# Optimization experiments

Hardware: AMD Instinct MI355X
Metric: run time of the kernel (lower is better)

## Reference

```python
import jax, jax.numpy as jnp
import numpy as np

N_SRC, N_DST, E, D, H = 100000, 10000, 320000, 128, 128
LN_EPS = 1e-5


def setup_inputs() -> dict:
    key = jax.random.key(0)
    ks = jax.random.split(key, 12)
    h_src = jax.random.normal(ks[0], (N_SRC, D), jnp.float32)
    h_dst = jax.random.normal(ks[1], (N_DST, D), jnp.float32)
    s_emb = jax.random.normal(ks[2], (N_DST, D), jnp.float32)
    edge_weight = jax.random.uniform(ks[3], (E,), jnp.float32)
    src_idx = jax.random.randint(ks[4], (E,), 0, N_SRC)
    dst_idx = jnp.sort(jax.random.randint(ks[5], (E,), 0, N_DST))
    # session_attention: Linear(2D->H, no bias) -> tanh -> Linear(H->1, no bias)
    W1 = jax.random.normal(ks[6], (2 * D, H), jnp.float32) / np.sqrt(2 * D)
    w2 = jax.random.normal(ks[7], (H,), jnp.float32) / np.sqrt(H)
    # output_proj: Linear(2D->D) with bias
    Wo = jax.random.normal(ks[8], (2 * D, D), jnp.float32) / np.sqrt(2 * D)
    bo = jnp.zeros((D,), jnp.float32)
    gamma = jnp.ones((D,), jnp.float32)
    beta = jnp.zeros((D,), jnp.float32)
    return {"h_src": h_src, "h_dst": h_dst, "s_emb": s_emb,
            "edge_weight": edge_weight, "src_idx": src_idx, "dst_idx": dst_idx,
            "W1": W1, "w2": w2, "Wo": Wo, "bo": bo, "gamma": gamma, "beta": beta}


def reference(h_src, h_dst, s_emb, edge_weight, src_idx, dst_idx, W1, w2, Wo, bo, gamma, beta):
    d = h_src.shape[1]
    # concat([h_src[src], s_emb[dst]]) @ W1 == h_src[src] @ W1[:d] + s_emb[dst] @ W1[d:]
    # project per-node first (cheaper than per-edge concat matmul)
    p_src = h_src @ W1[:d]          # [N_src, H]
    p_dst = s_emb @ W1[d:]          # [N_dst, H]
    raw = jnp.tanh(p_src[src_idx] + p_dst[dst_idx]) @ w2   # [E]
    raw = raw * edge_weight
    # edge_softmax: segment softmax over incoming edges of each dst node
    seg_max = jax.ops.segment_max(raw, dst_idx, num_segments=h_dst.shape[0])
    seg_max = jnp.where(jnp.isfinite(seg_max), seg_max, 0.0)  # handle degree-0 dsts
    ex = jnp.exp(raw - seg_max[dst_idx])
    den = jax.ops.segment_sum(ex, dst_idx, num_segments=h_dst.shape[0])
    attn = ex / den[dst_idx]                                 # [E]
    # u_mul_e + sum: weighted gather-scatter aggregation
    h_global = jax.ops.segment_sum(h_src[src_idx] * attn[:, None], dst_idx,
                                   num_segments=h_dst.shape[0])  # [N_dst, D]
    # output_proj on concat([h_dst, h_global])
    out = h_dst @ Wo[:d] + h_global @ Wo[d:] + bo
    # residual + layer norm (dropout = identity in eval)
    x = h_dst + out
    mu = jnp.mean(x, axis=-1, keepdims=True)
    var = jnp.mean((x - mu) ** 2, axis=-1, keepdims=True)
    y = (x - mu) / jnp.sqrt(var + LN_EPS) * gamma + beta
    return (y, attn[:, None])
```

## Files before the change

kernel.cpp:

```cpp
#include <hip/hip_runtime.h>
#include <math.h>

#define D128 128
#define SCAPW 256

typedef unsigned int uint32;
typedef unsigned short ushort_t;
typedef short bf16x8 __attribute__((ext_vector_type(8)));
typedef float f32x4 __attribute__((ext_vector_type(4)));
typedef float f32x2 __attribute__((ext_vector_type(2)));

__device__ __forceinline__ ushort_t bf16_of(float x) {
  uint32 u = __float_as_uint(x);
  return (ushort_t)((u + 0x7fffu + ((u >> 16) & 1u)) >> 16);
}
__device__ __forceinline__ uint32 pack_bf2(float x, float y) {
  uint32 bx = __float_as_uint(x);
  uint32 by = __float_as_uint(y);
  bx = (bx + 0x7fffu + ((bx >> 16) & 1u)) >> 16;
  by = (by + 0x7fffu + ((by >> 16) & 1u)) & 0xffff0000u;
  return bx | by;
}

__device__ __forceinline__ float fast_tanh(float x) {
  float e = __expf(2.0f * x);
  float r = __builtin_amdgcn_rcpf(1.0f + e);
  return fmaf(-2.0f, r, 1.0f);
}

__device__ __forceinline__ uint32 pack_fp8x4(float a, float b, float c, float d) {
  int u = __builtin_amdgcn_cvt_pk_fp8_f32(a, b, 0, false);
  u = __builtin_amdgcn_cvt_pk_fp8_f32(c, d, u, true);
  return (uint32)u;
}

__device__ __forceinline__ bf16x8 bf16x8_of(float4 a, float4 c) {
  union { uint4 u; bf16x8 h; } r;
  r.u.x = pack_bf2(a.x, a.y);
  r.u.y = pack_bf2(a.z, a.w);
  r.u.z = pack_bf2(c.x, c.y);
  r.u.w = pack_bf2(c.z, c.w);
  return r.h;
}

__device__ __forceinline__ float score8(uint2 us, f32x2 pd0, f32x2 pd1, f32x2 pd2,
                                        f32x2 pd3, float4 wA, float4 wB) {
  f32x2 a0 = __builtin_amdgcn_cvt_pk_f32_fp8(us.x, false);
  f32x2 a1 = __builtin_amdgcn_cvt_pk_f32_fp8(us.x, true);
  f32x2 a2 = __builtin_amdgcn_cvt_pk_f32_fp8(us.y, false);
  f32x2 a3 = __builtin_amdgcn_cvt_pk_f32_fp8(us.y, true);
  float sc;
  sc = fast_tanh(a0.x + pd0.x) * wA.x;
  sc = fmaf(fast_tanh(a0.y + pd0.y), wA.y, sc);
  sc = fmaf(fast_tanh(a1.x + pd1.x), wA.z, sc);
  sc = fmaf(fast_tanh(a1.y + pd1.y), wA.w, sc);
  sc = fmaf(fast_tanh(a2.x + pd2.x), wB.x, sc);
  sc = fmaf(fast_tanh(a2.y + pd2.y), wB.y, sc);
  sc = fmaf(fast_tanh(a3.x + pd3.x), wB.z, sc);
  sc = fmaf(fast_tanh(a3.y + pd3.y), wB.w, sc);
  return sc;
}

__global__ __launch_bounds__(256) void prep_all(
    const float* __restrict__ W1, const float* __restrict__ Wo,
    const int* __restrict__ dst_idx,
    ushort_t* __restrict__ Wfrag, ushort_t* __restrict__ Wo_frag,
    int* __restrict__ off, int E, int N) {
  const int b = blockIdx.x;
  const int tid = threadIdx.x;
  if (b < 16) {
    int t = b * 256 + tid;
    int lane = t & 63;
    int kc = (t >> 6) & 3;
    int nt = (t >> 8) & 7;
    int h = (t >> 11) & 1;
    int m = lane & 15;
    int quad = lane >> 4;
    int krow = h * D128 + kc * 32 + quad * 8;
    int ncol = nt * 16 + m;
    ushort_t fr[8];
#pragma unroll
    for (int j = 0; j < 8; j++) fr[j] = bf16_of(W1[(size_t)(krow + j) * D128 + ncol]);
    *(uint4*)(Wfrag + (size_t)t * 8) = *(const uint4*)fr;
  } else if (b < 32) {
    int t = (b - 16) * 256 + tid;
    int lane = t & 63;
    int kc = (t >> 6) & 7;
    int nt = (t >> 9) & 7;
    int m = lane & 15;
    int quad = lane >> 4;
    int krow = kc * 32 + quad * 8;
    int ncol = nt * 16 + m;
    ushort_t fr[8];
#pragma unroll
    for (int j = 0; j < 8; j++) fr[j] = bf16_of(Wo[(size_t)(krow + j) * D128 + ncol]);
    *(uint4*)(Wo_frag + (size_t)t * 8) = *(const uint4*)fr;
  } else {
    int e = (b - 32) * 256 + tid;
    if (e >= E) return;
    int d = dst_idx[e];
    int dprev = (e == 0) ? -1 : dst_idx[e - 1];
    for (int v = dprev + 1; v <= d; v++) off[v] = e;
    if (e == E - 1) {
      for (int v = d + 1; v <= N; v++) off[v] = E;
    }
  }
}

__global__ __launch_bounds__(256) void gemm_mfma(
    const float* __restrict__ Xa, const float* __restrict__ Xb,
    const ushort_t* __restrict__ Wfrag,
    uint32* __restrict__ Pa, uint32* __restrict__ Pb,
    uint32* __restrict__ x_f8,
    int Ma, int Mb, int nblk_a) {
  __shared__ uint4 WL[2048];
  const int blk = blockIdx.x;
  const float* X;
  const uint4* Wg;
  uint32* P;
  int M, row0;
  bool emit8;
  if (blk < nblk_a) {
    X = Xa; P = Pa; Wg = (const uint4*)Wfrag;             M = Ma; row0 = blk * 64; emit8 = true;
  } else {
    X = Xb; P = Pb; Wg = (const uint4*)(Wfrag + 16384);   M = Mb; row0 = (blk - nblk_a) * 64; emit8 = false;
  }

  const int tid = threadIdx.x;
  const int wave = tid >> 6;
  const int lane = tid & 63;
  const int m = lane & 15;
  const int quad = lane >> 4;

  const int ra = min(row0 + wave * 16 + m, M - 1);
  const float* xp = X + (size_t)ra * D128 + quad * 8;

  float4 xf[8];
#pragma unroll
  for (int kc = 0; kc < 4; kc++) {
    xf[kc * 2]     = *(const float4*)(xp + kc * 32);
    xf[kc * 2 + 1] = *(const float4*)(xp + kc * 32 + 4);
  }

  uint4 wtmp[8];
#pragma unroll
  for (int j = 0; j < 8; j++) wtmp[j] = Wg[tid + 256 * j];
#pragma unroll
  for (int j = 0; j < 8; j++) WL[tid + 256 * j] = wtmp[j];

  if (emit8) {
#pragma unroll
    for (int kc = 0; kc < 4; kc++) {
      uint2 q;
      q.x = pack_fp8x4(xf[kc * 2].x, xf[kc * 2].y, xf[kc * 2].z, xf[kc * 2].w);
      q.y = pack_fp8x4(xf[kc * 2 + 1].x, xf[kc * 2 + 1].y, xf[kc * 2 + 1].z, xf[kc * 2 + 1].w);
      *(uint2*)(x_f8 + (size_t)ra * 32 + kc * 8 + quad * 2) = q;
    }
  }
  bf16x8 xb[4];
#pragma unroll
  for (int kc = 0; kc < 4; kc++) xb[kc] = bf16x8_of(xf[kc * 2], xf[kc * 2 + 1]);

  __syncthreads();

  f32x4 acc[8];
#pragma unroll
  for (int nt = 0; nt < 8; nt++) acc[nt] = (f32x4){0.f, 0.f, 0.f, 0.f};

#pragma unroll
  for (int kc = 0; kc < 4; kc++) {
#pragma unroll
    for (int nt = 0; nt < 8; nt++) {
      bf16x8 wf = *(const bf16x8*)&WL[(nt * 4 + kc) * 64 + lane];
      acc[nt] = __builtin_amdgcn_mfma_f32_16x16x32_bf16(wf, xb[kc], acc[nt], 0, 0, 0);
    }
  }

  __syncthreads();
  uint32* Ys = (uint32*)WL;
#pragma unroll
  for (int nt = 0; nt < 8; nt++)
    Ys[(wave * 16 + m) * 36 + nt * 4 + quad] =
        pack_fp8x4(acc[nt][0], acc[nt][1], acc[nt][2], acc[nt][3]);
  __syncthreads();

#pragma unroll
  for (int it = 0; it < 2; it++) {
    int f = tid + 256 * it;
    int row = f >> 3;
    int cu = (f & 7) * 4;
    int grow = row0 + row;
    if (grow < M) *(uint4*)(P + (size_t)grow * 32 + cu) = *(const uint4*)(&Ys[row * 36 + cu]);
  }
}

__global__ __launch_bounds__(256) void attn_agg_kernel(
    const uint32* __restrict__ p_src_f8, const uint32* __restrict__ p_dst_f8,
    const float* __restrict__ w2, const float* __restrict__ ew,
    const int* __restrict__ src_idx, const int* __restrict__ off,
    const uint32* __restrict__ h_src_f8,
    float* __restrict__ attn_out, uint32* __restrict__ h_glob_bf, int N_dst) {
  const int tid = threadIdx.x;
  const int wv = tid >> 6;
  const int lane = tid & 63;
  const int v = blockIdx.x * 4 + wv;

  __shared__ float sex[4][SCAPW];
  __shared__ int ssrc[4][SCAPW];
  if (v >= N_dst) return;

  const int lo = off[v], hi = off[v + 1];
  const int deg = hi - lo;
  const int sub = lane & 15;
  const int eg = lane >> 4;
  const bool fast = (deg <= SCAPW);

  float4 wA = *(const float4*)(w2 + sub * 8);
  float4 wB = *(const float4*)(w2 + sub * 8 + 4);
  uint2 pdu = *(const uint2*)(p_dst_f8 + (size_t)v * 32 + sub * 2);
  f32x2 pd0 = __builtin_amdgcn_cvt_pk_f32_fp8(pdu.x, false);
  f32x2 pd1 = __builtin_amdgcn_cvt_pk_f32_fp8(pdu.x, true);
  f32x2 pd2 = __builtin_amdgcn_cvt_pk_f32_fp8(pdu.y, false);
  f32x2 pd3 = __builtin_amdgcn_cvt_pk_f32_fp8(pdu.y, true);

  float den = 0.f;
  for (int base = 0; base < deg; base += 8) {
    const int ei0 = base + eg;
    const int ei1 = base + 4 + eg;
    const bool v0 = ei0 < deg;
    const bool v1 = ei1 < deg;
    int s0 = 0, s1 = 0;
    float ew0 = 0.f, ew1 = 0.f;
    uint2 us0, us1;
    us0.x = us0.y = us1.x = us1.y = 0u;
    if (v0) {
      const int e = lo + ei0;
      s0 = src_idx[e];
      ew0 = ew[e];
      us0 = *(const uint2*)(p_src_f8 + (size_t)s0 * 32 + sub * 2);
    }
    if (v1) {
      const int e = lo + ei1;
      s1 = src_idx[e];
      ew1 = ew[e];
      us1 = *(const uint2*)(p_src_f8 + (size_t)s1 * 32 + sub * 2);
    }
    float ex0 = 0.f, ex1 = 0.f;
    if (v0) {
      float sc = score8(us0, pd0, pd1, pd2, pd3, wA, wB);
#pragma unroll
      for (int o = 1; o <= 8; o <<= 1) sc += __shfl_xor(sc, o, 64);
      ex0 = __expf(sc * ew0);
      if (sub == 0) {
        if (fast) { sex[wv][ei0] = ex0; ssrc[wv][ei0] = s0; }
        else attn_out[lo + ei0] = ex0;
      }
    }
    if (v1) {
      float sc = score8(us1, pd0, pd1, pd2, pd3, wA, wB);
#pragma unroll
      for (int o = 1; o <= 8; o <<= 1) sc += __shfl_xor(sc, o, 64);
      ex1 = __expf(sc * ew1);
      if (sub == 0) {
        if (fast) { sex[wv][ei1] = ex1; ssrc[wv][ei1] = s1; }
        else attn_out[lo + ei1] = ex1;
      }
    }
    den += (sub == 0) ? (ex0 + ex1) : 0.f;
  }
#pragma unroll
  for (int o = 1; o <= 32; o <<= 1) den += __shfl_xor(den, o, 64);
  const float inv = (deg > 0) ? 1.0f / den : 0.0f;

  const int c4 = lane & 31;
  const int hw = lane >> 5;
  float a0 = 0.f, a1 = 0.f, a2 = 0.f, a3 = 0.f;

  if (fast) {
    const int pad = (deg + 15) & ~15;
    for (int i = deg + lane; i < pad; i += 64) { sex[wv][i] = 0.f; ssrc[wv][i] = 0; }
    for (int i = lane; i < deg; i += 64) attn_out[lo + i] = sex[wv][i] * inv;
    for (int b = 0; b < pad; b += 16) {
#pragma unroll
      for (int j = 0; j < 8; j++) {
        const int idx = b + j * 2 + hw;
        float ex = sex[wv][idx];
        int s = ssrc[wv][idx];
        uint32 u = h_src_f8[(size_t)s * 32 + c4];
        f32x2 h0 = __builtin_amdgcn_cvt_pk_f32_fp8(u, false);
        f32x2 h1 = __builtin_amdgcn_cvt_pk_f32_fp8(u, true);
        a0 = fmaf(ex, h0.x, a0);
        a1 = fmaf(ex, h0.y, a1);
        a2 = fmaf(ex, h1.x, a2);
        a3 = fmaf(ex, h1.y, a3);
      }
    }
  } else {
    for (int b = 0; b < deg; b += 16) {
#pragma unroll
      for (int j = 0; j < 8; j++) {
        const int idx = b + j * 2 + hw;
        float ex = 0.f;
        int s = 0;
        if (idx < deg) { ex = attn_out[lo + idx]; s = src_idx[lo + idx]; }
        uint32 u = h_src_f8[(size_t)s * 32 + c4];
        f32x2 h0 = __builtin_amdgcn_cvt_pk_f32_fp8(u, false);
        f32x2 h1 = __builtin_amdgcn_cvt_pk_f32_fp8(u, true);
        a0 = fmaf(ex, h0.x, a0);
        a1 = fmaf(ex, h0.y, a1);
        a2 = fmaf(ex, h1.x, a2);
        a3 = fmaf(ex, h1.y, a3);
      }
    }
    for (int i = lane; i < deg; i += 64) attn_out[lo + i] *= inv;
  }

  a0 += __shfl_xor(a0, 32, 64);
  a1 += __shfl_xor(a1, 32, 64);
  a2 += __shfl_xor(a2, 32, 64);
  a3 += __shfl_xor(a3, 32, 64);
  if (hw == 0) {
    uint2 o;
    o.x = pack_bf2(a0 * inv, a1 * inv);
    o.y = pack_bf2(a2 * inv, a3 * inv);
    *(uint2*)(h_glob_bf + (size_t)v * 64 + c4 * 2) = o;
  }
}

__global__ __launch_bounds__(128) void out_mfma_ln(
    const float* __restrict__ h_dst, const ushort_t* __restrict__ h_glob_bf,
    const ushort_t* __restrict__ Wo_frag,
    const float* __restrict__ bo,
    const float* __restrict__ gamma, const float* __restrict__ beta,
    float* __restrict__ y, int N) {
  __shared__ float sbo[128], sgam[128], sbet[128];
  const int tid = threadIdx.x;
  if (tid < 128) { sbo[tid] = bo[tid]; sgam[tid] = gamma[tid]; sbet[tid] = beta[tid]; }
  __syncthreads();

  const int w = tid >> 6;
  const int lane = tid & 63;
  const int m = lane & 15;
  const int quad = lane >> 4;
  const int row0 = blockIdx.x * 32 + w * 16;
  const int ra = min(row0 + m, N - 1);
  const bf16x8* Wf = (const bf16x8*)Wo_frag;

  float4 f0[4], f1[4];
  bf16x8 ag[4];
#pragma unroll
  for (int kc = 0; kc < 4; kc++) {
    const float* p = h_dst + (size_t)ra * D128 + kc * 32 + quad * 8;
    f0[kc] = *(const float4*)p;
    f1[kc] = *(const float4*)(p + 4);
  }
#pragma unroll
  for (int kc = 0; kc < 4; kc++)
    ag[kc] = *(const bf16x8*)(h_glob_bf + (size_t)ra * D128 + kc * 32 + quad * 8);

  f32x4 acc[8];
#pragma unroll
  for (int nt = 0; nt < 8; nt++) acc[nt] = (f32x4){0.f, 0.f, 0.f, 0.f};

#pragma unroll
  for (int kc = 0; kc < 8; kc++) {
    bf16x8 a = (kc < 4) ? bf16x8_of(f0[kc & 3], f1[kc & 3]) : ag[kc & 3];
#pragma unroll
    for (int nt = 0; nt < 8; nt++) {
      bf16x8 bfr = Wf[(nt * 8 + kc) * 64 + lane];
      acc[nt] = __builtin_amdgcn_mfma_f32_16x16x32_bf16(a, bfr, acc[nt], 0, 0, 0);
    }
  }

#pragma unroll
  for (int r = 0; r < 4; r++) {
    const int grow = row0 + quad * 4 + r;
    const int gr = min(grow, N - 1);
    float x[8];
    float s1 = 0.f, s2 = 0.f;
#pragma unroll
    for (int nt = 0; nt < 8; nt++) {
      float hd = h_dst[(size_t)gr * D128 + nt * 16 + m];
      float xv = hd + acc[nt][r] + sbo[nt * 16 + m];
      x[nt] = xv;
      s1 += xv;
      s2 = fmaf(xv, xv, s2);
    }
#pragma unroll
    for (int o = 1; o <= 8; o <<= 1) {
      s1 += __shfl_xor(s1, o, 64);
      s2 += __shfl_xor(s2, o, 64);
    }
    float mu = s1 * (1.0f / 128.0f);
    float var = s2 * (1.0f / 128.0f) - mu * mu;
    float rstd = __builtin_amdgcn_rcpf(sqrtf(var + 1e-5f));
    if (grow < N) {
#pragma unroll
      for (int nt = 0; nt < 8; nt++) {
        int c = nt * 16 + m;
        y[(size_t)grow * D128 + c] = (x[nt] - mu) * rstd * sgam[c] + sbet[c];
      }
    }
  }
}

extern "C" void kernel_launch(void* const* d_in, const int* in_sizes, int n_in,
                              void* d_out, int out_size, void* d_ws, size_t ws_size,
                              hipStream_t stream) {
  const float* h_src = (const float*)d_in[0];
  const float* h_dst = (const float*)d_in[1];
  const float* s_emb = (const float*)d_in[2];
  const float* ew    = (const float*)d_in[3];
  const int* src_idx = (const int*)d_in[4];
  const int* dst_idx = (const int*)d_in[5];
  const float* W1    = (const float*)d_in[6];
  const float* w2    = (const float*)d_in[7];
  const float* Wo    = (const float*)d_in[8];
  const float* bo    = (const float*)d_in[9];
  const float* gamma = (const float*)d_in[10];
  const float* beta  = (const float*)d_in[11];

  const int N_src = in_sizes[0] / D128;
  const int N_dst = in_sizes[1] / D128;
  const int E = in_sizes[3];

  float* out_y = (float*)d_out;
  float* out_attn = out_y + (size_t)N_dst * D128;

  uint32* p_src_f8 = (uint32*)d_ws;
  uint32* p_dst_f8 = p_src_f8 + (size_t)N_src * 32;
  uint32* h_src_f8 = p_dst_f8 + (size_t)N_dst * 32;
  uint32* h_glob_bf = h_src_f8 + (size_t)N_src * 32;
  int* seg_off = (int*)(h_glob_bf + (size_t)N_dst * 64);
  ushort_t* Wfrag = (ushort_t*)(seg_off + N_dst + 1 + 3);
  ushort_t* Wo_frag = Wfrag + 32768;

  const int nblk_a = (N_src + 63) / 64;
  const int nblk_b = (N_dst + 63) / 64;
  const int nb_seg = (E + 255) / 256;

  prep_all<<<32 + nb_seg, 256, 0, stream>>>(
      W1, Wo, dst_idx, Wfrag, Wo_frag, seg_off, E, N_dst);
  gemm_mfma<<<nblk_a + nblk_b, 256, 0, stream>>>(
      h_src, s_emb, Wfrag, p_src_f8, p_dst_f8, h_src_f8, N_src, N_dst, nblk_a);
  attn_agg_kernel<<<(N_dst + 3) / 4, 256, 0, stream>>>(
      p_src_f8, p_dst_f8, w2, ew, src_idx, seg_off, h_src_f8, out_attn,
      h_glob_bf, N_dst);
  out_mfma_ln<<<(N_dst + 31) / 32, 128, 0, stream>>>(
      h_dst, (const ushort_t*)h_glob_bf, Wo_frag,
      bo, gamma, beta, out_y, N_dst);
}
```

Baseline: 163.0 us.

## Split edge scoring into edge-parallel kernel and stage Wo fragments in LDS

Edge attention scoring moves out of the per-destination aggregation kernel into a separate edge-parallel kernel, so that load balance no longer depends on node degree. The aggregation kernel then reads the exp scores back from global memory to form the denominator and weighted sum. This adds one kernel launch and an extra round trip of the scores through global memory. Separately, the output projection now uses 256-thread blocks that stage the two halves of the Wo fragments in shared memory, with the fragment layout reordered to match.

```diff
diff --git a/kernel.cpp b/kernel.cpp
--- a/kernel.cpp
+++ b/kernel.cpp
@@ -2,7 +2,6 @@
 #include <math.h>
 
 #define D128 128
-#define SCAPW 256
 
 typedef unsigned int uint32;
 typedef unsigned short ushort_t;
@@ -43,21 +42,24 @@
   return r.h;
 }
 
-__device__ __forceinline__ float score8(uint2 us, f32x2 pd0, f32x2 pd1, f32x2 pd2,
-                                        f32x2 pd3, float4 wA, float4 wB) {
+__device__ __forceinline__ float score8_raw(uint2 us, uint2 ud, float4 wA, float4 wB) {
   f32x2 a0 = __builtin_amdgcn_cvt_pk_f32_fp8(us.x, false);
   f32x2 a1 = __builtin_amdgcn_cvt_pk_f32_fp8(us.x, true);
   f32x2 a2 = __builtin_amdgcn_cvt_pk_f32_fp8(us.y, false);
   f32x2 a3 = __builtin_amdgcn_cvt_pk_f32_fp8(us.y, true);
+  f32x2 d0 = __builtin_amdgcn_cvt_pk_f32_fp8(ud.x, false);
+  f32x2 d1 = __builtin_amdgcn_cvt_pk_f32_fp8(ud.x, true);
+  f32x2 d2 = __builtin_amdgcn_cvt_pk_f32_fp8(ud.y, false);
+  f32x2 d3 = __builtin_amdgcn_cvt_pk_f32_fp8(ud.y, true);
   float sc;
-  sc = fast_tanh(a0.x + pd0.x) * wA.x;
-  sc = fmaf(fast_tanh(a0.y + pd0.y), wA.y, sc);
-  sc = fmaf(fast_tanh(a1.x + pd1.x), wA.z, sc);
-  sc = fmaf(fast_tanh(a1.y + pd1.y), wA.w, sc);
-  sc = fmaf(fast_tanh(a2.x + pd2.x), wB.x, sc);
-  sc = fmaf(fast_tanh(a2.y + pd2.y), wB.y, sc);
-  sc = fmaf(fast_tanh(a3.x + pd3.x), wB.z, sc);
-  sc = fmaf(fast_tanh(a3.y + pd3.y), wB.w, sc);
+  sc = fast_tanh(a0.x + d0.x) * wA.x;
+  sc = fmaf(fast_tanh(a0.y + d0.y), wA.y, sc);
+  sc = fmaf(fast_tanh(a1.x + d1.x), wA.z, sc);
+  sc = fmaf(fast_tanh(a1.y + d1.y), wA.w, sc);
+  sc = fmaf(fast_tanh(a2.x + d2.x), wB.x, sc);
+  sc = fmaf(fast_tanh(a2.y + d2.y), wB.y, sc);
+  sc = fmaf(fast_tanh(a3.x + d3.x), wB.z, sc);
+  sc = fmaf(fast_tanh(a3.y + d3.y), wB.w, sc);
   return sc;
 }
 
@@ -85,11 +87,12 @@
   } else if (b < 32) {
     int t = (b - 16) * 256 + tid;
     int lane = t & 63;
-    int kc = (t >> 6) & 7;
-    int nt = (t >> 9) & 7;
+    int kc4 = (t >> 6) & 3;
+    int nt = (t >> 8) & 7;
+    int half = (t >> 11) & 1;
     int m = lane & 15;
     int quad = lane >> 4;
-    int krow = kc * 32 + quad * 8;
+    int krow = (half * 4 + kc4) * 32 + quad * 8;
     int ncol = nt * 16 + m;
     ushort_t fr[8];
 #pragma unroll
@@ -194,9 +197,47 @@
   }
 }
 
-__global__ __launch_bounds__(256) void attn_agg_kernel(
+__global__ __launch_bounds__(256) void score_kernel(
     const uint32* __restrict__ p_src_f8, const uint32* __restrict__ p_dst_f8,
     const float* __restrict__ w2, const float* __restrict__ ew,
+    const int* __restrict__ src_idx, const int* __restrict__ dst_idx,
+    float* __restrict__ ex_out, int E) {
+  const int tid = threadIdx.x;
+  const int wv = tid >> 6;
+  const int lane = tid & 63;
+  const int sub = lane & 15;
+  const int eg = lane >> 4;
+  const int wbase = (blockIdx.x * 4 + wv) * 64;
+  if (wbase >= E) return;
+
+  const float4 wA = *(const float4*)(w2 + sub * 8);
+  const float4 wB = *(const float4*)(w2 + sub * 8 + 4);
+
+  for (int i0 = 0; i0 < 64; i0 += 16) {
+    int e[4];
+    uint2 us[4], ud[4];
+    float ewv[4];
+#pragma unroll
+    for (int j = 0; j < 4; j++) {
+      e[j] = wbase + i0 + j * 4 + eg;
+      const int ee = min(e[j], E - 1);
+      const int s = src_idx[ee];
+      const int d = dst_idx[ee];
+      ewv[j] = ew[ee];
+      us[j] = *(const uint2*)(p_src_f8 + (size_t)s * 32 + sub * 2);
+      ud[j] = *(const uint2*)(p_dst_f8 + (size_t)d * 32 + sub * 2);
+    }
+#pragma unroll
+    for (int j = 0; j < 4; j++) {
+      float sc = score8_raw(us[j], ud[j], wA, wB);
+#pragma unroll
+      for (int o = 1; o <= 8; o <<= 1) sc += __shfl_xor(sc, o, 64);
+      if (sub == 0 && e[j] < E) ex_out[e[j]] = __expf(sc * ewv[j]);
+    }
+  }
+}
+
+__global__ __launch_bounds__(256) void agg_kernel(
     const int* __restrict__ src_idx, const int* __restrict__ off,
     const uint32* __restrict__ h_src_f8,
     float* __restrict__ attn_out, uint32* __restrict__ h_glob_bf, int N_dst) {
@@ -204,70 +245,13 @@
   const int wv = tid >> 6;
   const int lane = tid & 63;
   const int v = blockIdx.x * 4 + wv;
-
-  __shared__ float sex[4][SCAPW];
-  __shared__ int ssrc[4][SCAPW];
   if (v >= N_dst) return;
 
   const int lo = off[v], hi = off[v + 1];
   const int deg = hi - lo;
-  const int sub = lane & 15;
-  const int eg = lane >> 4;
-  const bool fast = (deg <= SCAPW);
-
-  float4 wA = *(const float4*)(w2 + sub * 8);
-  float4 wB = *(const float4*)(w2 + sub * 8 + 4);
-  uint2 pdu = *(const uint2*)(p_dst_f8 + (size_t)v * 32 + sub * 2);
-  f32x2 pd0 = __builtin_amdgcn_cvt_pk_f32_fp8(pdu.x, false);
-  f32x2 pd1 = __builtin_amdgcn_cvt_pk_f32_fp8(pdu.x, true);
-  f32x2 pd2 = __builtin_amdgcn_cvt_pk_f32_fp8(pdu.y, false);
-  f32x2 pd3 = __builtin_amdgcn_cvt_pk_f32_fp8(pdu.y, true);
 
   float den = 0.f;
-  for (int base = 0; base < deg; base += 8) {
-    const int ei0 = base + eg;
-    const int ei1 = base + 4 + eg;
-    const bool v0 = ei0 < deg;
-    const bool v1 = ei1 < deg;
-    int s0 = 0, s1 = 0;
-    float ew0 = 0.f, ew1 = 0.f;
-    uint2 us0, us1;
-    us0.x = us0.y = us1.x = us1.y = 0u;
-    if (v0) {
-      const int e = lo + ei0;
-      s0 = src_idx[e];
-      ew0 = ew[e];
-      us0 = *(const uint2*)(p_src_f8 + (size_t)s0 * 32 + sub * 2);
-    }
-    if (v1) {
-      const int e = lo + ei1;
-      s1 = src_idx[e];
-      ew1 = ew[e];
-      us1 = *(const uint2*)(p_src_f8 + (size_t)s1 * 32 + sub * 2);
-    }
-    float ex0 = 0.f, ex1 = 0.f;
-    if (v0) {
-      float sc = score8(us0, pd0, pd1, pd2, pd3, wA, wB);
-#pragma unroll
-      for (int o = 1; o <= 8; o <<= 1) sc += __shfl_xor(sc, o, 64);
-      ex0 = __expf(sc * ew0);
-      if (sub == 0) {
-        if (fast) { sex[wv][ei0] = ex0; ssrc[wv][ei0] = s0; }
-        else attn_out[lo + ei0] = ex0;
-      }
-    }
-    if (v1) {
-      float sc = score8(us1, pd0, pd1, pd2, pd3, wA, wB);
-#pragma unroll
-      for (int o = 1; o <= 8; o <<= 1) sc += __shfl_xor(sc, o, 64);
-      ex1 = __expf(sc * ew1);
-      if (sub == 0) {
-        if (fast) { sex[wv][ei1] = ex1; ssrc[wv][ei1] = s1; }
-        else attn_out[lo + ei1] = ex1;
-      }
-    }
-    den += (sub == 0) ? (ex0 + ex1) : 0.f;
-  }
+  for (int i = lane; i < deg; i += 64) den += attn_out[lo + i];
 #pragma unroll
   for (int o = 1; o <= 32; o <<= 1) den += __shfl_xor(den, o, 64);
   const float inv = (deg > 0) ? 1.0f / den : 0.0f;
@@ -276,44 +260,23 @@
   const int hw = lane >> 5;
   float a0 = 0.f, a1 = 0.f, a2 = 0.f, a3 = 0.f;
 
-  if (fast) {
-    const int pad = (deg + 15) & ~15;
-    for (int i = deg + lane; i < pad; i += 64) { sex[wv][i] = 0.f; ssrc[wv][i] = 0; }
-    for (int i = lane; i < deg; i += 64) attn_out[lo + i] = sex[wv][i] * inv;
-    for (int b = 0; b < pad; b += 16) {
-#pragma unroll
-      for (int j = 0; j < 8; j++) {
-        const int idx = b + j * 2 + hw;
-        float ex = sex[wv][idx];
-        int s = ssrc[wv][idx];
-        uint32 u = h_src_f8[(size_t)s * 32 + c4];
-        f32x2 h0 = __builtin_amdgcn_cvt_pk_f32_fp8(u, false);
-        f32x2 h1 = __builtin_amdgcn_cvt_pk_f32_fp8(u, true);
-        a0 = fmaf(ex, h0.x, a0);
-        a1 = fmaf(ex, h0.y, a1);
-        a2 = fmaf(ex, h1.x, a2);
-        a3 = fmaf(ex, h1.y, a3);
-      }
-    }
-  } else {
-    for (int b = 0; b < deg; b += 16) {
-#pragma unroll
-      for (int j = 0; j < 8; j++) {
-        const int idx = b + j * 2 + hw;
-        float ex = 0.f;
-        int s = 0;
-        if (idx < deg) { ex = attn_out[lo + idx]; s = src_idx[lo + idx]; }
-        uint32 u = h_src_f8[(size_t)s * 32 + c4];
-        f32x2 h0 = __builtin_amdgcn_cvt_pk_f32_fp8(u, false);
-        f32x2 h1 = __builtin_amdgcn_cvt_pk_f32_fp8(u, true);
-        a0 = fmaf(ex, h0.x, a0);
-        a1 = fmaf(ex, h0.y, a1);
-        a2 = fmaf(ex, h1.x, a2);
-        a3 = fmaf(ex, h1.y, a3);
-      }
-    }
-    for (int i = lane; i < deg; i += 64) attn_out[lo + i] *= inv;
-  }
+  for (int b = 0; b < deg; b += 16) {
+#pragma unroll
+    for (int j = 0; j < 8; j++) {
+      const int idx = b + j * 2 + hw;
+      float ex = 0.f;
+      int s = 0;
+      if (idx < deg) { ex = attn_out[lo + idx]; s = src_idx[lo + idx]; }
+      uint32 u = h_src_f8[(size_t)s * 32 + c4];
+      f32x2 h0 = __builtin_amdgcn_cvt_pk_f32_fp8(u, false);
+      f32x2 h1 = __builtin_amdgcn_cvt_pk_f32_fp8(u, true);
+      a0 = fmaf(ex, h0.x, a0);
+      a1 = fmaf(ex, h0.y, a1);
+      a2 = fmaf(ex, h1.x, a2);
+      a3 = fmaf(ex, h1.y, a3);
+    }
+  }
+  for (int i = lane; i < deg; i += 64) attn_out[lo + i] *= inv;
 
   a0 += __shfl_xor(a0, 32, 64);
   a1 += __shfl_xor(a1, 32, 64);
@@ -327,24 +290,30 @@
   }
 }
 
-__global__ __launch_bounds__(128) void out_mfma_ln(
+__global__ __launch_bounds__(256) void out_mfma_ln(
     const float* __restrict__ h_dst, const ushort_t* __restrict__ h_glob_bf,
     const ushort_t* __restrict__ Wo_frag,
     const float* __restrict__ bo,
     const float* __restrict__ gamma, const float* __restrict__ beta,
     float* __restrict__ y, int N) {
+  __shared__ uint4 WL[2048];
   __shared__ float sbo[128], sgam[128], sbet[128];
   const int tid = threadIdx.x;
   if (tid < 128) { sbo[tid] = bo[tid]; sgam[tid] = gamma[tid]; sbet[tid] = beta[tid]; }
-  __syncthreads();
 
   const int w = tid >> 6;
   const int lane = tid & 63;
   const int m = lane & 15;
   const int quad = lane >> 4;
-  const int row0 = blockIdx.x * 32 + w * 16;
+  const int row0 = blockIdx.x * 64 + w * 16;
   const int ra = min(row0 + m, N - 1);
-  const bf16x8* Wf = (const bf16x8*)Wo_frag;
+  const uint4* Wg = (const uint4*)Wo_frag;
+
+  uint4 wt0[8], wt1[8];
+#pragma unroll
+  for (int j = 0; j < 8; j++) wt0[j] = Wg[tid + 256 * j];
+#pragma unroll
+  for (int j = 0; j < 8; j++) wt1[j] = Wg[2048 + tid + 256 * j];
 
   float4 f0[4], f1[4];
   bf16x8 ag[4];
@@ -363,11 +332,28 @@
   for (int nt = 0; nt < 8; nt++) acc[nt] = (f32x4){0.f, 0.f, 0.f, 0.f};
 
 #pragma unroll
-  for (int kc = 0; kc < 8; kc++) {
-    bf16x8 a = (kc < 4) ? bf16x8_of(f0[kc & 3], f1[kc & 3]) : ag[kc & 3];
+  for (int j = 0; j < 8; j++) WL[tid + 256 * j] = wt0[j];
+  __syncthreads();
+#pragma unroll
+  for (int kc = 0; kc < 4; kc++) {
+    bf16x8 a = bf16x8_of(f0[kc], f1[kc]);
 #pragma unroll
     for (int nt = 0; nt < 8; nt++) {
-      bf16x8 bfr = Wf[(nt * 8 + kc) * 64 + lane];
+      bf16x8 bfr = *(const bf16x8*)&WL[(nt * 4 + kc) * 64 + lane];
+      acc[nt] = __builtin_amdgcn_mfma_f32_16x16x32_bf16(a, bfr, acc[nt], 0, 0, 0);
+    }
+  }
+  __syncthreads();
+
+#pragma unroll
+  for (int j = 0; j < 8; j++) WL[tid + 256 * j] = wt1[j];
+  __syncthreads();
+#pragma unroll
+  for (int kc = 0; kc < 4; kc++) {
+    bf16x8 a = ag[kc];
+#pragma unroll
+    for (int nt = 0; nt < 8; nt++) {
+      bf16x8 bfr = *(const bf16x8*)&WL[(nt * 4 + kc) * 64 + lane];
       acc[nt] = __builtin_amdgcn_mfma_f32_16x16x32_bf16(a, bfr, acc[nt], 0, 0, 0);
     }
   }
@@ -443,10 +429,11 @@
       W1, Wo, dst_idx, Wfrag, Wo_frag, seg_off, E, N_dst);
   gemm_mfma<<<nblk_a + nblk_b, 256, 0, stream>>>(
       h_src, s_emb, Wfrag, p_src_f8, p_dst_f8, h_src_f8, N_src, N_dst, nblk_a);
-  attn_agg_kernel<<<(N_dst + 3) / 4, 256, 0, stream>>>(
-      p_src_f8, p_dst_f8, w2, ew, src_idx, seg_off, h_src_f8, out_attn,
-      h_glob_bf, N_dst);
-  out_mfma_ln<<<(N_dst + 31) / 32, 128, 0, stream>>>(
+  score_kernel<<<(E + 255) / 256, 256, 0, stream>>>(
+      p_src_f8, p_dst_f8, w2, ew, src_idx, dst_idx, out_attn, E);
+  agg_kernel<<<(N_dst + 3) / 4, 256, 0, stream>>>(
+      src_idx, seg_off, h_src_f8, out_attn, h_glob_bf, N_dst);
+  out_mfma_ln<<<(N_dst + 63) / 64, 256, 0, stream>>>(
       h_dst, (const ushort_t*)h_glob_bf, Wo_frag,
       bo, gamma, beta, out_y, N_dst);
 }
```

Measured after the change: 171.4 us. +5.2%, slower.
